# Kernel tuning notes

Measured on AMD Instinct MI355X. Metric: run time of the kernel, lower is better.

## Reference

```python
import jax, jax.numpy as jnp
import numpy as np

B, T, H, L, C = 128, 2048, 256, 2, 7


def _lstm_layer(x, W_ih, W_hh, b_ih, b_hh):
    # x: [B, T, I]; W_ih: [4H, I]; W_hh: [4H, H]
    h_dim = W_hh.shape[1]
    # precompute input contribution for all timesteps
    xg = jnp.einsum('bti,gi->btg', x, W_ih) + b_ih + b_hh  # [B, T, 4H]
    xg_t = jnp.swapaxes(xg, 0, 1)  # [T, B, 4H]

    def step(carry, g_in):
        h, c = carry
        g = g_in + h @ W_hh.T  # [B, 4H]
        i, f, gg, o = jnp.split(g, 4, axis=-1)  # PyTorch gate order i,f,g,o
        i = jax.nn.sigmoid(i)
        f = jax.nn.sigmoid(f)
        gg = jnp.tanh(gg)
        o = jax.nn.sigmoid(o)
        c = f * c + i * gg
        h = o * jnp.tanh(c)
        return (h, c), h

    h0 = jnp.zeros((x.shape[0], h_dim), x.dtype)
    c0 = jnp.zeros((x.shape[0], h_dim), x.dtype)
    _, hs = jax.lax.scan(step, (h0, c0), xg_t)  # [T, B, H]
    return jnp.swapaxes(hs, 0, 1)  # [B, T, H]


def setup_inputs() -> dict:
    key = jax.random.key(0)
    ks = jax.random.split(key, 12)
    s0 = 1.0  # init scale ~ 1/sqrt(H) applied below
    sc = 1.0 / np.sqrt(H)
    inp = {
        'x': jax.random.normal(ks[0], (B, T, 1), dtype=jnp.float32),
        'lengths': jax.random.randint(ks[1], (B,), 1, T + 1, dtype=jnp.int32),
        'W_ih0': jax.random.normal(ks[2], (4 * H, 1), dtype=jnp.float32) * sc,
        'W_hh0': jax.random.normal(ks[3], (4 * H, H), dtype=jnp.float32) * sc,
        'b_ih0': jax.random.normal(ks[4], (4 * H,), dtype=jnp.float32) * sc,
        'b_hh0': jax.random.normal(ks[5], (4 * H,), dtype=jnp.float32) * sc,
        'W_ih1': jax.random.normal(ks[6], (4 * H, H), dtype=jnp.float32) * sc,
        'W_hh1': jax.random.normal(ks[7], (4 * H, H), dtype=jnp.float32) * sc,
        'b_ih1': jax.random.normal(ks[8], (4 * H,), dtype=jnp.float32) * sc,
        'b_hh1': jax.random.normal(ks[9], (4 * H,), dtype=jnp.float32) * sc,
        'W_lin': jax.random.normal(ks[10], (C, H), dtype=jnp.float32) * sc,
        'b_lin': jax.random.normal(ks[11], (C,), dtype=jnp.float32) * sc,
    }
    return inp


def reference(x, lengths, W_ih0, W_hh0, b_ih0, b_hh0, W_ih1, W_hh1, b_ih1, b_hh1, W_lin, b_lin):
    # 2-layer LSTM (batch_first). Padded positions are computed but never read,
    # because the masked mean only covers t < lengths[b] (matches PackedSequence math).
    h1 = _lstm_layer(x, W_ih0, W_hh0, b_ih0, b_hh0)   # [B, T, H]
    h2 = _lstm_layer(h1, W_ih1, W_hh1, b_ih1, b_hh1)  # [B, T, H]
    # per-sample variable-length mean pooling (vectorized segment mean)
    t_idx = jnp.arange(h2.shape[1])
    mask = (t_idx[None, :] < lengths[:, None]).astype(h2.dtype)  # [B, T]
    pooled = jnp.einsum('bth,bt->bh', h2, mask) / lengths[:, None].astype(h2.dtype)
    return pooled @ W_lin.T + b_lin  # [B, C]
```

## Files before the change

### kernel.cpp

```cpp
#include <hip/hip_runtime.h>
#include <stdint.h>

#define TT 2048
#define HH 256
#define BB 128

typedef __attribute__((ext_vector_type(8))) short short8;
typedef __attribute__((ext_vector_type(4))) float f32x4;

__device__ __forceinline__ unsigned short f2bf(float f) {
  union { float f; unsigned int u; } v; v.f = f;
  unsigned int r = v.u + 0x7fffu + ((v.u >> 16) & 1u);
  return (unsigned short)(r >> 16);
}
__device__ __forceinline__ float sigm(float x) { return 1.0f / (1.0f + __expf(-x)); }
__device__ __forceinline__ float tanh_f(float x) { return 1.0f - 2.0f / (1.0f + __expf(2.0f * x)); }

__device__ __forceinline__ void mfma_a(f32x4& acc, short8 a, short8 b) {
  asm("v_mfma_f32_16x16x32_bf16 %0, %1, %2, %0" : "+v"(acc) : "v"(a), "a"(b));
}
__device__ __forceinline__ void mfma_v(f32x4& acc, short8 a, short8 b) {
  asm("v_mfma_f32_16x16x32_bf16 %0, %1, %2, %0" : "+v"(acc) : "v"(a), "v"(b));
}
__device__ __forceinline__ short8 ld16_ic(const unsigned short* p) {
  union { unsigned long long q[2]; short8 v; } u;
  u.q[0] = __hip_atomic_load((const unsigned long long*)p, __ATOMIC_RELAXED, __HIP_MEMORY_SCOPE_AGENT);
  u.q[1] = __hip_atomic_load(((const unsigned long long*)p) + 1, __ATOMIC_RELAXED, __HIP_MEMORY_SCOPE_AGENT);
  return u.v;
}
__device__ __forceinline__ void st2_ic(unsigned short* p, unsigned short v) {
  unsigned int vv = v;
  asm volatile("global_store_short %0, %1, off sc0 sc1" :: "v"(p), "v"(vv) : "memory");
}
__device__ __forceinline__ void vmcnt0() { asm volatile("s_waitcnt vmcnt(0)" ::: "memory"); }
__device__ __forceinline__ void waitN(int* f, int idx, int tgt) {
  for (;;) {
    int v = __hip_atomic_load(&f[idx * 16], __ATOMIC_RELAXED, __HIP_MEMORY_SCOPE_AGENT);
    if (__all(v >= tgt)) break;
    __builtin_amdgcn_s_sleep(1);
  }
}

__global__ void prep_kernel(const float* __restrict__ whh0, const float* __restrict__ wih1,
                            const float* __restrict__ whh1,
                            const float* __restrict__ bih0, const float* __restrict__ bhh0,
                            const float* __restrict__ bih1, const float* __restrict__ bhh1,
                            unsigned short* __restrict__ whh0b, unsigned short* __restrict__ wih1b,
                            unsigned short* __restrict__ whh1b,
                            float* __restrict__ bsum0, float* __restrict__ bsum1,
                            int* __restrict__ flags) {
  int i = blockIdx.x * blockDim.x + threadIdx.x;
  if (i < 262144) {
    whh0b[i] = f2bf(whh0[i]);
    wih1b[i] = f2bf(wih1[i]);
    whh1b[i] = f2bf(whh1[i]);
  }
  if (i < 1024) bsum0[i] = bih0[i] + bhh0[i];
  else if (i < 2048) { int j = i - 1024; bsum1[j] = bih1[j] + bhh1[j]; }
  if (i < 8192) flags[i] = 0;
}

__attribute__((amdgpu_flat_work_group_size(256, 256)))
__attribute__((amdgpu_waves_per_eu(1, 1)))
__global__ void rec_all(
    const float* __restrict__ x,
    const unsigned short* __restrict__ whh0b, const float* __restrict__ wih0,
    const float* __restrict__ bsum0,
    const unsigned short* __restrict__ wih1b,
    const unsigned short* __restrict__ whh1b, const float* __restrict__ bsum1,
    const int* __restrict__ lengths,
    float* __restrict__ pooled,
    unsigned short* __restrict__ h1ring,
    unsigned short* __restrict__ h2ring,
    int* flags)
{
  const int tid = threadIdx.x;
  const int lane = tid & 63;
  const int w = tid >> 6;
  const int l15 = lane & 15, l4 = lane >> 4;
  const int isL1 = (blockIdx.x >= 32);
  const int wg = blockIdx.x & 31;
  const int q = wg >> 3;
  const int bg = wg & 7;
  const int b0 = bg * 16;
  const int unit = q * 64 + w * 16 + l15;
  const int myfid = (int)blockIdx.x * 4 + w;

  const unsigned short* WH = isL1 ? whh1b : whh0b;
  short8 wfh[4][8];
#pragma unroll
  for (int gt = 0; gt < 4; ++gt)
#pragma unroll
    for (int kk = 0; kk < 8; ++kk)
      wfh[gt][kk] = *(const short8*)(WH + (size_t)(gt * 256 + unit) * 256 + kk * 32 + l4 * 8);
  short8 wfi[4][8];
  if (isL1) {
#pragma unroll
    for (int gt = 0; gt < 4; ++gt)
#pragma unroll
      for (int kk = 0; kk < 8; ++kk)
        wfi[gt][kk] = *(const short8*)(wih1b + (size_t)(gt * 256 + unit) * 256 + kk * 32 + l4 * 8);
  }
  float bs_l[4], wih0_l[4];
#pragma unroll
  for (int gt = 0; gt < 4; ++gt) {
    bs_l[gt] = (isL1 ? bsum1 : bsum0)[gt * 256 + unit];
    wih0_l[gt] = isL1 ? 0.0f : wih0[gt * 256 + unit];
  }

  float c_[4] = {0.f, 0.f, 0.f, 0.f};
  float psum[4] = {0.f, 0.f, 0.f, 0.f};
  int len_[4];
#pragma unroll
  for (int r = 0; r < 4; ++r) len_[r] = lengths[b0 + l4 * 4 + r];

  for (int t = 0; t < TT; ++t) {
    {
      int idx = myfid, tgt = 0;
      if (!isL1) {
        if (lane < 16) {
          if (t > 0) { idx = ((lane >> 2) * 8 + bg) * 4 + (lane & 3); tgt = t; }
        } else if (lane < 32) {
          if (t >= 8 && (t & 3) == 0) {
            idx = 128 + (((lane - 16) >> 2) * 8 + bg) * 4 + (lane & 3); tgt = t - 4;
          }
        }
      } else {
        if (lane < 16) { idx = ((lane >> 2) * 8 + bg) * 4 + (lane & 3); tgt = t + 1; }
        else if (lane < 32) {
          if (t > 0) { idx = 128 + (((lane - 16) >> 2) * 8 + bg) * 4 + (lane & 3); tgt = t; }
        }
      }
      waitN(flags, idx, tgt);
    }

    f32x4 z = {0.f, 0.f, 0.f, 0.f};
    f32x4 acc[4];
#pragma unroll
    for (int gt = 0; gt < 4; ++gt) acc[gt] = z;

    if (!isL1) {
      if (t > 0) {
        const unsigned short* hrow = h1ring + ((size_t)((t - 1) & 7) * BB + b0 + l15) * HH;
        short8 af[8];
#pragma unroll
        for (int kk = 0; kk < 8; ++kk) af[kk] = ld16_ic(hrow + kk * 32 + l4 * 8);
#pragma unroll
        for (int gt = 0; gt < 4; ++gt)
#pragma unroll
          for (int kk = 0; kk < 8; ++kk) mfma_a(acc[gt], af[kk], wfh[gt][kk]);
      }
#pragma unroll
      for (int r = 0; r < 4; ++r) {
        const int sr = l4 * 4 + r;
        const float xv = x[(size_t)(b0 + sr) * TT + t];
        float pi = acc[0][r] + bs_l[0] + xv * wih0_l[0];
        float pf = acc[1][r] + bs_l[1] + xv * wih0_l[1];
        float pg = acc[2][r] + bs_l[2] + xv * wih0_l[2];
        float po = acc[3][r] + bs_l[3] + xv * wih0_l[3];
        const float ig = sigm(pi), fg = sigm(pf), gg = tanh_f(pg), og = sigm(po);
        const float cn = fg * c_[r] + ig * gg;
        c_[r] = cn;
        const float hn = og * tanh_f(cn);
        st2_ic(&h1ring[((size_t)(t & 7) * BB + b0 + sr) * HH + unit], f2bf(hn));
      }
    } else {
      short8 af1[8], af2[8];
      {
        const unsigned short* h1row = h1ring + ((size_t)(t & 7) * BB + b0 + l15) * HH;
#pragma unroll
        for (int kk = 0; kk < 8; ++kk) af1[kk] = ld16_ic(h1row + kk * 32 + l4 * 8);
      }
      if (t > 0) {
        const unsigned short* h2row = h2ring + ((size_t)((t - 1) & 1) * BB + b0 + l15) * HH;
#pragma unroll
        for (int kk = 0; kk < 8; ++kk) af2[kk] = ld16_ic(h2row + kk * 32 + l4 * 8);
      }
#pragma unroll
      for (int gt = 0; gt < 4; ++gt)
#pragma unroll
        for (int kk = 0; kk < 8; ++kk) mfma_v(acc[gt], af1[kk], wfi[gt][kk]);
      if (t > 0) {
#pragma unroll
        for (int gt = 0; gt < 4; ++gt)
#pragma unroll
          for (int kk = 0; kk < 8; ++kk) mfma_a(acc[gt], af2[kk], wfh[gt][kk]);
      }
#pragma unroll
      for (int r = 0; r < 4; ++r) {
        const int sr = l4 * 4 + r;
        float pi = acc[0][r] + bs_l[0];
        float pf = acc[1][r] + bs_l[1];
        float pg = acc[2][r] + bs_l[2];
        float po = acc[3][r] + bs_l[3];
        const float ig = sigm(pi), fg = sigm(pf), gg = tanh_f(pg), og = sigm(po);
        const float cn = fg * c_[r] + ig * gg;
        c_[r] = cn;
        const float hn = og * tanh_f(cn);
        st2_ic(&h2ring[((size_t)(t & 1) * BB + b0 + sr) * HH + unit], f2bf(hn));
        if (t < len_[r]) psum[r] += hn;
      }
    }

    vmcnt0();
    if (lane == 0)
      __hip_atomic_store(&flags[myfid * 16], t + 1, __ATOMIC_RELAXED, __HIP_MEMORY_SCOPE_AGENT);
  }

  if (isL1) {
#pragma unroll
    for (int r = 0; r < 4; ++r)
      pooled[(size_t)(b0 + l4 * 4 + r) * HH + unit] = psum[r];
  }
}

__global__ void out_kernel(const float* __restrict__ pooled, const int* __restrict__ lengths,
                           const float* __restrict__ wlin, const float* __restrict__ blin,
                           float* __restrict__ out) {
  const int b = blockIdx.x;
  const int lane = threadIdx.x;
  float s[7];
#pragma unroll
  for (int c = 0; c < 7; ++c) s[c] = 0.f;
  for (int k = lane; k < 256; k += 64) {
    const float pv = pooled[b * 256 + k];
#pragma unroll
    for (int c = 0; c < 7; ++c) s[c] += pv * wlin[c * 256 + k];
  }
#pragma unroll
  for (int c = 0; c < 7; ++c) {
#pragma unroll
    for (int off = 32; off > 0; off >>= 1) s[c] += __shfl_down(s[c], off);
  }
  if (lane == 0) {
    const float inv = 1.0f / (float)lengths[b];
#pragma unroll
    for (int c = 0; c < 7; ++c) out[b * 7 + c] = s[c] * inv + blin[c];
  }
}

extern "C" void kernel_launch(void* const* d_in, const int* in_sizes, int n_in,
                              void* d_out, int out_size, void* d_ws, size_t ws_size,
                              hipStream_t stream) {
  const float* x      = (const float*)d_in[0];
  const int*   lengths= (const int*)d_in[1];
  const float* W_ih0  = (const float*)d_in[2];
  const float* W_hh0  = (const float*)d_in[3];
  const float* b_ih0  = (const float*)d_in[4];
  const float* b_hh0  = (const float*)d_in[5];
  const float* W_ih1  = (const float*)d_in[6];
  const float* W_hh1  = (const float*)d_in[7];
  const float* b_ih1  = (const float*)d_in[8];
  const float* b_hh1  = (const float*)d_in[9];
  const float* W_lin  = (const float*)d_in[10];
  const float* b_lin  = (const float*)d_in[11];
  float* out = (float*)d_out;

  char* ws = (char*)d_ws;
  unsigned short* whh0b = (unsigned short*)(ws + 0);
  unsigned short* wih1b = (unsigned short*)(ws + 524288);
  unsigned short* whh1b = (unsigned short*)(ws + 1048576);
  float* bsum0   = (float*)(ws + 1572864);
  float* bsum1   = (float*)(ws + 1576960);
  int*   flags   = (int*)  (ws + 1581056);
  float* pooled  = (float*)(ws + 1613824);
  unsigned short* h2ring = (unsigned short*)(ws + 1744896);
  unsigned short* h1ring = (unsigned short*)(ws + 1875968);

  prep_kernel<<<dim3(1024), dim3(256), 0, stream>>>(
      W_hh0, W_ih1, W_hh1, b_ih0, b_hh0, b_ih1, b_hh1,
      whh0b, wih1b, whh1b, bsum0, bsum1, flags);

  rec_all<<<dim3(64), dim3(256), 0, stream>>>(
      x, whh0b, W_ih0, bsum0, wih1b, whh1b, bsum1, lengths,
      pooled, h1ring, h2ring, flags);

  out_kernel<<<dim3(128), dim3(64), 0, stream>>>(pooled, lengths, W_lin, b_lin, out);
}
```

Before: 11.47 ms.

## Overlap flag polling with flag publish and drop sleep in spin-wait

Moves the cross-block dependency wait from the start of each timestep to the end of the previous one. A relaxed poll load of the next step's producer flags is issued before this block publishes its own flag. Polling uses two loads kept in flight alternately, with explicit vmcnt waits and no s_sleep. The aim is to shorten the per-step handoff latency in the serial recurrence, at the cost of more spinning memory traffic and reliance on hand-ordered waitcnt semantics for store visibility.

```diff
diff --git a/kernel.cpp b/kernel.cpp
--- a/kernel.cpp
+++ b/kernel.cpp
@@ -32,7 +32,6 @@
   unsigned int vv = v;
   asm volatile("global_store_short %0, %1, off sc0 sc1" :: "v"(p), "v"(vv) : "memory");
 }
-__device__ __forceinline__ void vmcnt0() { asm volatile("s_waitcnt vmcnt(0)" ::: "memory"); }
 __device__ __forceinline__ void waitN(int* f, int idx, int tgt) {
   for (;;) {
     int v = __hip_atomic_load(&f[idx * 16], __ATOMIC_RELAXED, __HIP_MEMORY_SCOPE_AGENT);
@@ -40,6 +39,11 @@
     __builtin_amdgcn_s_sleep(1);
   }
 }
+#define POLL(dst, ptr) \
+  asm volatile("global_load_dword %0, %1, off sc0 sc1" : "=v"(dst) : "v"(ptr) : "memory")
+#define VMW(n) \
+  do { asm volatile("s_waitcnt vmcnt(" #n ")" ::: "memory"); \
+       __builtin_amdgcn_sched_barrier(0); } while (0)
 
 __global__ void prep_kernel(const float* __restrict__ whh0, const float* __restrict__ wih1,
                             const float* __restrict__ whh1,
@@ -114,26 +118,14 @@
 #pragma unroll
   for (int r = 0; r < 4; ++r) len_[r] = lengths[b0 + l4 * 4 + r];
 
+  if (isL1) {
+    int idx = myfid, tgt = 0;
+    if (lane < 16) { idx = ((lane >> 2) * 8 + bg) * 4 + (lane & 3); tgt = 1; }
+    waitN(flags, idx, tgt);
+  }
+
+  int pa, pb;
   for (int t = 0; t < TT; ++t) {
-    {
-      int idx = myfid, tgt = 0;
-      if (!isL1) {
-        if (lane < 16) {
-          if (t > 0) { idx = ((lane >> 2) * 8 + bg) * 4 + (lane & 3); tgt = t; }
-        } else if (lane < 32) {
-          if (t >= 8 && (t & 3) == 0) {
-            idx = 128 + (((lane - 16) >> 2) * 8 + bg) * 4 + (lane & 3); tgt = t - 4;
-          }
-        }
-      } else {
-        if (lane < 16) { idx = ((lane >> 2) * 8 + bg) * 4 + (lane & 3); tgt = t + 1; }
-        else if (lane < 32) {
-          if (t > 0) { idx = 128 + (((lane - 16) >> 2) * 8 + bg) * 4 + (lane & 3); tgt = t; }
-        }
-      }
-      waitN(flags, idx, tgt);
-    }
-
     f32x4 z = {0.f, 0.f, 0.f, 0.f};
     f32x4 acc[4];
 #pragma unroll
@@ -202,9 +194,43 @@
       }
     }
 
-    vmcnt0();
-    if (lane == 0)
-      __hip_atomic_store(&flags[myfid * 16], t + 1, __ATOMIC_RELAXED, __HIP_MEMORY_SCOPE_AGENT);
+    {
+      const int s = t + 1;
+      int idx = myfid, tgt = 0;
+      if (!isL1) {
+        if (lane < 16) { idx = ((lane >> 2) * 8 + bg) * 4 + (lane & 3); tgt = s; }
+        else if (lane < 32) {
+          if (s >= 8 && (s & 3) == 0) {
+            idx = 128 + (((lane - 16) >> 2) * 8 + bg) * 4 + (lane & 3); tgt = s - 4;
+          }
+        }
+      } else {
+        if (lane < 16) { idx = ((lane >> 2) * 8 + bg) * 4 + (lane & 3); tgt = s + 1; }
+        else if (lane < 32) { idx = 128 + (((lane - 16) >> 2) * 8 + bg) * 4 + (lane & 3); tgt = s; }
+      }
+      const int* pp = &flags[idx * 16];
+
+      POLL(pa, pp);
+      VMW(1);
+      if (lane == 0)
+        __hip_atomic_store(&flags[myfid * 16], s, __ATOMIC_RELAXED, __HIP_MEMORY_SCOPE_AGENT);
+      if (s < TT) {
+        POLL(pb, pp);
+        VMW(2);
+        if (!__all(pa >= tgt)) {
+          POLL(pa, pp);
+          VMW(1);
+          for (;;) {
+            if (__all(pb >= tgt)) break;
+            POLL(pb, pp);
+            VMW(1);
+            if (__all(pa >= tgt)) break;
+            POLL(pa, pp);
+            VMW(1);
+          }
+        }
+      }
+    }
   }
 
   if (isL1) {
```

After: 13.16 ms. 14.7% more time.
